# Kernel optimization log

Hardware: AMD Instinct MI355X
Metric: run time of the kernel (lower is better)

## Reference

```python
import jax, jax.numpy as jnp
import numpy as np

N_NODES = 100000
N_EDGES = 1600000


def setup_inputs() -> dict:
    key = jax.random.key(0)
    k1, k2, k3, k4 = jax.random.split(key, 4)
    x = jax.random.normal(k1, (N_NODES, 128), dtype=jnp.float32)
    edge_idx = jax.random.randint(k2, (2, N_EDGES), 0, N_NODES, dtype=jnp.int64)
    W1 = jax.random.normal(k3, (128, 64), dtype=jnp.float32) * (1.0 / np.sqrt(128))
    b1 = jnp.zeros((64,), dtype=jnp.float32)
    W2 = jax.random.normal(k4, (64, 40), dtype=jnp.float32) * (1.0 / np.sqrt(64))
    b2 = jnp.zeros((40,), dtype=jnp.float32)
    return {"x": x, "edge_idx": edge_idx, "W1": W1, "b1": b1, "W2": W2, "b2": b2}


def _gcn_conv(x, src, dst, norm, W, b, n_nodes):
    # x @ W -> gather by src, scale by symmetric norm, scatter-add to dst, + bias
    h = x @ W                               # [N, d_out]
    msg = h[src] * norm[:, None]            # [E+N, d_out]
    out = jax.ops.segment_sum(msg, dst, num_segments=n_nodes)
    return out + b


def _norm_and_loops(edge_idx, n_nodes):
    # PyG GCNConv default: add self-loops, norm = deg^-1/2[src] * deg^-1/2[dst]
    loops = jnp.arange(n_nodes, dtype=edge_idx.dtype)
    src = jnp.concatenate([edge_idx[0], loops])
    dst = jnp.concatenate([edge_idx[1], loops])
    deg = jnp.zeros((n_nodes,), jnp.float32).at[dst].add(1.0)
    dinv = jnp.where(deg > 0, jax.lax.rsqrt(deg), 0.0)
    norm = dinv[src] * dinv[dst]
    return src, dst, norm


def reference(x, edge_idx, W1, b1, W2, b2):
    n_nodes = x.shape[0]
    src, dst, norm = _norm_and_loops(edge_idx, n_nodes)
    hidden = jax.nn.relu(_gcn_conv(x, src, dst, norm, W1, b1, n_nodes))
    # dropout is a no-op in eval mode (training=False)
    return _gcn_conv(hidden, src, dst, norm, W2, b2, n_nodes)
```

## Files before the change

kernel.cpp:

```cpp
#include <hip/hip_runtime.h>

#define D_IN  128
#define D_HID 64
#define D_OUT 40

static __device__ __forceinline__ unsigned short f2bf(float f) {
    unsigned int u = __float_as_uint(f);
    unsigned int r = (u + 0x7fffu + ((u >> 16) & 1u)) >> 16;
    return (unsigned short)r;
}
static __device__ __forceinline__ float bflo(unsigned int u) {
    return __uint_as_float(u << 16);
}
static __device__ __forceinline__ float bfhi(unsigned int u) {
    return __uint_as_float(u & 0xffff0000u);
}

__global__ __launch_bounds__(256) void k_deg_g1(const int* __restrict__ dst,
                                                unsigned int* __restrict__ cnt,
                                                unsigned int* __restrict__ rank, int E, int DB,
                                                const float* __restrict__ x,
                                                const float* __restrict__ W1,
                                                unsigned short* __restrict__ h1s, int N) {
    __shared__ float w[D_IN * D_HID];
    __shared__ float xs[16][D_IN + 4];
    if ((int)blockIdx.x < DB) {
        int e = blockIdx.x * 256 + threadIdx.x;
        if (e < E) rank[e] = atomicAdd(&cnt[dst[e]], 1u);
        return;
    }
    const int tid = threadIdx.x;
    const float4* W4 = (const float4*)W1;
    float4* w4 = (float4*)w;
    for (int i = tid; i < D_IN * D_HID / 4; i += 256) w4[i] = W4[i];
    const int row0 = (blockIdx.x - DB) * 16;
    const float4* X4 = (const float4*)(x + (size_t)row0 * D_IN);
    for (int i = tid; i < 16 * D_IN / 4; i += 256) {
        float4 v = X4[i];
        int r = i >> 5;
        int k = (i & 31) * 4;
        *(float4*)&xs[r][k] = v;
    }
    __syncthreads();
    const int r  = tid >> 4;
    const int c4 = (tid & 15) * 4;
    float a0 = 0, a1 = 0, a2 = 0, a3 = 0;
#pragma unroll 8
    for (int k = 0; k < D_IN; ++k) {
        float  xv = xs[r][k];
        float4 wv = *(const float4*)&w[k * D_HID + c4];
        a0 = fmaf(xv, wv.x, a0);
        a1 = fmaf(xv, wv.y, a1);
        a2 = fmaf(xv, wv.z, a2);
        a3 = fmaf(xv, wv.w, a3);
    }
    const int row = row0 + r;
    if (row < N) {
        uint2 o;
        o.x = (unsigned)f2bf(a0) | ((unsigned)f2bf(a1) << 16);
        o.y = (unsigned)f2bf(a2) | ((unsigned)f2bf(a3) << 16);
        *(uint2*)&h1s[(size_t)row * D_HID + c4] = o;
    }
}

__global__ __launch_bounds__(256) void k_scan1(const unsigned int* __restrict__ deg,
                                               unsigned int* __restrict__ off,
                                               unsigned int* __restrict__ bsum,
                                               float* __restrict__ dinv, int N) {
    __shared__ unsigned int s[256];
    const int tid = threadIdx.x;
    const int i = blockIdx.x * 256 + tid;
    unsigned int v = (i < N) ? deg[i] : 0u;
    if (i < N) dinv[i] = rsqrtf((float)(v + 1u));
    s[tid] = v;
    __syncthreads();
    for (int d = 1; d < 256; d <<= 1) {
        unsigned int t = (tid >= d) ? s[tid - d] : 0u;
        __syncthreads();
        s[tid] += t;
        __syncthreads();
    }
    if (i < N) off[i] = s[tid] - v;
    if (tid == 255) bsum[blockIdx.x] = s[tid];
}

__global__ __launch_bounds__(512) void k_scan2(unsigned int* __restrict__ bsum, int NB) {
    __shared__ unsigned int s[512];
    const int tid = threadIdx.x;
    unsigned int v = (tid < NB) ? bsum[tid] : 0u;
    s[tid] = v;
    __syncthreads();
    for (int d = 1; d < 512; d <<= 1) {
        unsigned int t = (tid >= d) ? s[tid - d] : 0u;
        __syncthreads();
        s[tid] += t;
        __syncthreads();
    }
    if (tid < NB) bsum[tid] = s[tid] - v;
}

__global__ __launch_bounds__(256) void k_scan3(unsigned int* __restrict__ off,
                                               const unsigned int* __restrict__ bsum,
                                               int N, int E) {
    int i = blockIdx.x * 256 + threadIdx.x;
    if (i < N) off[i] += bsum[blockIdx.x];
    if (i == 0) off[N] = (unsigned int)E;
}

__global__ __launch_bounds__(256) void k_fill(const int* __restrict__ src,
                                              const int* __restrict__ dst,
                                              const unsigned int* __restrict__ off,
                                              const unsigned int* __restrict__ rank,
                                              int* __restrict__ csr_src, int E) {
    int e = blockIdx.x * 256 + threadIdx.x;
    if (e >= E) return;
    csr_src[off[dst[e]] + rank[e]] = src[e];
}

__global__ __launch_bounds__(256) void k_g1g2(const unsigned int* __restrict__ off,
                                              const int* __restrict__ csr_src,
                                              const unsigned int* __restrict__ h1s,
                                              const float* __restrict__ dinv,
                                              const float* __restrict__ b1,
                                              const float* __restrict__ W2,
                                              unsigned short* __restrict__ h2s, int N) {
    __shared__ float w2s[D_HID * D_OUT];
    __shared__ float hrow[8][D_HID];
    const int tid = threadIdx.x;
    const float4* W4 = (const float4*)W2;
    float4* w4 = (float4*)w2s;
    for (int i = tid; i < D_HID * D_OUT / 4; i += 256) w4[i] = W4[i];
    __syncthreads();

    const int lane = tid & 63;
    const int half = lane >> 5;
    const int hl   = lane & 31;
    const int slot = (tid >> 6) * 2 + half;
    const int node = blockIdx.x * 8 + slot;
    const bool valid = node < N;

    int start = 0, end = 0;
    float a0 = 0.0f, a1 = 0.0f;
    float dn = 0.0f;
    if (valid) {
        start = (int)off[node];
        end   = (int)off[node + 1];
        dn = dinv[node];
        unsigned int u = h1s[(size_t)node * 32 + hl];
        a0 = dn * bflo(u);
        a1 = dn * bfhi(u);
    }
    for (int base = start; base < end; base += 32) {
        const int nb = min(32, end - base);
        int sv = (base + hl < end) ? csr_src[base + hl] : 0;
        int j = 0;
        for (; j + 3 < nb; j += 4) {
            int s0 = __shfl(sv, j, 32),     s1 = __shfl(sv, j + 1, 32);
            int s2 = __shfl(sv, j + 2, 32), s3 = __shfl(sv, j + 3, 32);
            unsigned int u0 = h1s[(size_t)s0 * 32 + hl]; float d0 = dinv[s0];
            unsigned int u1 = h1s[(size_t)s1 * 32 + hl]; float d1 = dinv[s1];
            unsigned int u2 = h1s[(size_t)s2 * 32 + hl]; float d2 = dinv[s2];
            unsigned int u3 = h1s[(size_t)s3 * 32 + hl]; float d3 = dinv[s3];
            a0 = fmaf(d0, bflo(u0), a0); a1 = fmaf(d0, bfhi(u0), a1);
            a0 = fmaf(d1, bflo(u1), a0); a1 = fmaf(d1, bfhi(u1), a1);
            a0 = fmaf(d2, bflo(u2), a0); a1 = fmaf(d2, bfhi(u2), a1);
            a0 = fmaf(d3, bflo(u3), a0); a1 = fmaf(d3, bfhi(u3), a1);
        }
        for (; j < nb; ++j) {
            int s = __shfl(sv, j, 32);
            unsigned int uu = h1s[(size_t)s * 32 + hl];
            float dd = dinv[s];
            a0 = fmaf(dd, bflo(uu), a0);
            a1 = fmaf(dd, bfhi(uu), a1);
        }
    }
    if (valid) {
        const float2 bb = *(const float2*)&b1[hl * 2];
        float v0 = fmaf(dn, a0, bb.x);
        float v1 = fmaf(dn, a1, bb.y);
        hrow[slot][hl * 2]     = v0 > 0.0f ? v0 : 0.0f;
        hrow[slot][hl * 2 + 1] = v1 > 0.0f ? v1 : 0.0f;
    }
    __syncthreads();
    if (valid && hl < 20) {
        const int c2 = hl * 2;
        float s0 = 0.0f, s1 = 0.0f;
#pragma unroll 8
        for (int k = 0; k < D_HID; ++k) {
            float  xv = hrow[slot][k];
            float2 wv = *(const float2*)&w2s[k * D_OUT + c2];
            s0 = fmaf(xv, wv.x, s0);
            s1 = fmaf(xv, wv.y, s1);
        }
        unsigned int o = (unsigned)f2bf(s0 * dn) | ((unsigned)f2bf(s1 * dn) << 16);
        *(unsigned int*)&h2s[(size_t)node * D_OUT + c2] = o;
    }
}

__global__ __launch_bounds__(256) void k_gather2(const unsigned int* __restrict__ off,
                                                 const int* __restrict__ csr_src,
                                                 const unsigned int* __restrict__ h2s,
                                                 const float* __restrict__ dinv,
                                                 const float* __restrict__ b2,
                                                 float* __restrict__ out, int N) {
    const int gtid = blockIdx.x * 256 + threadIdx.x;
    const int wid2 = gtid >> 6;
    const int lane = threadIdx.x & 63;
    const int half = lane >> 5;
    const int hl   = lane & 31;
    const int node = wid2 * 2 + half;
    if (node >= N) return;
    const int start = (int)off[node];
    const int end   = (int)off[node + 1];
    const bool act = hl < 20;
    float a0 = 0.0f, a1 = 0.0f;
    if (act) {
        unsigned int u = h2s[(size_t)node * 20 + hl];
        a0 = bflo(u); a1 = bfhi(u);
    }
    for (int base = start; base < end; base += 32) {
        const int nb = min(32, end - base);
        int sv = (base + hl < end) ? csr_src[base + hl] : 0;
        int j = 0;
        for (; j + 3 < nb; j += 4) {
            int s0 = __shfl(sv, j, 32),     s1 = __shfl(sv, j + 1, 32);
            int s2 = __shfl(sv, j + 2, 32), s3 = __shfl(sv, j + 3, 32);
            if (act) {
                unsigned int u0 = h2s[(size_t)s0 * 20 + hl];
                unsigned int u1 = h2s[(size_t)s1 * 20 + hl];
                unsigned int u2 = h2s[(size_t)s2 * 20 + hl];
                unsigned int u3 = h2s[(size_t)s3 * 20 + hl];
                a0 += (bflo(u0) + bflo(u1)) + (bflo(u2) + bflo(u3));
                a1 += (bfhi(u0) + bfhi(u1)) + (bfhi(u2) + bfhi(u3));
            }
        }
        for (; j < nb; ++j) {
            int s = __shfl(sv, j, 32);
            if (act) {
                unsigned int uu = h2s[(size_t)s * 20 + hl];
                a0 += bflo(uu);
                a1 += bfhi(uu);
            }
        }
    }
    if (act) {
        const float dv = dinv[node];
        const float2 bb = *(const float2*)&b2[hl * 2];
        float2 o = {fmaf(dv, a0, bb.x), fmaf(dv, a1, bb.y)};
        *(float2*)&out[(size_t)node * D_OUT + hl * 2] = o;
    }
}

extern "C" void kernel_launch(void* const* d_in, const int* in_sizes, int n_in,
                              void* d_out, int out_size, void* d_ws, size_t ws_size,
                              hipStream_t stream) {
    const float* x  = (const float*)d_in[0];
    const int*  eix = (const int*)d_in[1];
    const float* W1 = (const float*)d_in[2];
    const float* b1 = (const float*)d_in[3];
    const float* W2 = (const float*)d_in[4];
    const float* b2 = (const float*)d_in[5];
    float* out = (float*)d_out;

    const int N = in_sizes[0] / D_IN;
    const int E = in_sizes[1] / 2;
    const int* src = eix;
    const int* dst = eix + E;
    const int NB = (N + 255) / 256;

    char* ws = (char*)d_ws;
    size_t off_b = 0;
    auto alloc = [&](size_t bytes) {
        void* p = ws + off_b;
        off_b = (off_b + bytes + 255) & ~(size_t)255;
        return p;
    };
    unsigned int*   deg     = (unsigned int*)alloc((size_t)N * 4);
    float*          dinv    = (float*)alloc((size_t)N * 4);
    unsigned int*   offsets = (unsigned int*)alloc((size_t)(N + 1) * 4);
    unsigned int*   bsums   = (unsigned int*)alloc(512 * 4);
    int*            csr_src = (int*)alloc((size_t)E * 4);
    unsigned short* h1s     = (unsigned short*)alloc((size_t)N * D_HID * 2);
    unsigned short* h2s     = (unsigned short*)alloc((size_t)E >= (size_t)N * D_OUT / 2
                                                     ? (size_t)E * 4 : (size_t)N * D_OUT * 2);
    unsigned int*   rank    = (unsigned int*)h2s;

    hipMemsetAsync(deg, 0, (size_t)N * 4, stream);

    const int DB = (E + 255) / 256;
    const int GB = (N + 15) / 16;

    k_deg_g1<<<DB + GB, 256, 0, stream>>>(dst, deg, rank, E, DB, x, W1, h1s, N);

    k_scan1<<<NB, 256, 0, stream>>>(deg, offsets, bsums, dinv, N);
    k_scan2<<<1, 512, 0, stream>>>(bsums, NB);
    k_scan3<<<NB, 256, 0, stream>>>(offsets, bsums, N, E);
    k_fill <<<(E + 255) / 256, 256, 0, stream>>>(src, dst, offsets, rank, csr_src, E);

    k_g1g2  <<<(N + 7) / 8, 256, 0, stream>>>(offsets, csr_src, (const unsigned int*)h1s,
                                              dinv, b1, W2, h2s, N);
    const int gwaves = (N + 1) / 2;
    const int gblocks = (gwaves + 3) / 4;
    k_gather2<<<gblocks, 256, 0, stream>>>(offsets, csr_src, (const unsigned int*)h2s,
                                           dinv, b2, out, N);
}
```

Measured before the change: 328.2 us.

## Prescale layer-1 features by source dinv to drop per-edge dinv gathers

The degree-count and GEMM1 kernels are split apart so GEMM1 runs after dinv is known. Each row of h1 is then multiplied by its source node's inverse-sqrt degree before the bf16 store. This removes the random per-edge dinv loads and multiplies from the layer-1 gather, which becomes a plain sum. The cost is losing the overlap of the atomic degree pass with the GEMM, plus a serialization point and a slight change in bf16 rounding.

Measured after the change: 338.1 us. 1.03x slower.

```diff
diff --git a/kernel.cpp b/kernel.cpp
--- a/kernel.cpp
+++ b/kernel.cpp
@@ -16,24 +16,78 @@
     return __uint_as_float(u & 0xffff0000u);
 }
 
-__global__ __launch_bounds__(256) void k_deg_g1(const int* __restrict__ dst,
-                                                unsigned int* __restrict__ cnt,
-                                                unsigned int* __restrict__ rank, int E, int DB,
-                                                const float* __restrict__ x,
-                                                const float* __restrict__ W1,
-                                                unsigned short* __restrict__ h1s, int N) {
+__global__ __launch_bounds__(256) void k_deg(const int* __restrict__ dst,
+                                             unsigned int* __restrict__ cnt,
+                                             unsigned int* __restrict__ rank, int E) {
+    int e = blockIdx.x * 256 + threadIdx.x;
+    if (e < E) rank[e] = atomicAdd(&cnt[dst[e]], 1u);
+}
+
+__global__ __launch_bounds__(256) void k_scan1(const unsigned int* __restrict__ deg,
+                                               unsigned int* __restrict__ off,
+                                               unsigned int* __restrict__ bsum,
+                                               float* __restrict__ dinv, int N) {
+    __shared__ unsigned int s[256];
+    const int tid = threadIdx.x;
+    const int i = blockIdx.x * 256 + tid;
+    unsigned int v = (i < N) ? deg[i] : 0u;
+    if (i < N) dinv[i] = rsqrtf((float)(v + 1u));
+    s[tid] = v;
+    __syncthreads();
+    for (int d = 1; d < 256; d <<= 1) {
+        unsigned int t = (tid >= d) ? s[tid - d] : 0u;
+        __syncthreads();
+        s[tid] += t;
+        __syncthreads();
+    }
+    if (i < N) off[i] = s[tid] - v;
+    if (tid == 255) bsum[blockIdx.x] = s[tid];
+}
+
+__global__ __launch_bounds__(512) void k_scan2(unsigned int* __restrict__ bsum, int NB) {
+    __shared__ unsigned int s[512];
+    const int tid = threadIdx.x;
+    unsigned int v = (tid < NB) ? bsum[tid] : 0u;
+    s[tid] = v;
+    __syncthreads();
+    for (int d = 1; d < 512; d <<= 1) {
+        unsigned int t = (tid >= d) ? s[tid - d] : 0u;
+        __syncthreads();
+        s[tid] += t;
+        __syncthreads();
+    }
+    if (tid < NB) bsum[tid] = s[tid] - v;
+}
+
+__global__ __launch_bounds__(256) void k_scan3(unsigned int* __restrict__ off,
+                                               const unsigned int* __restrict__ bsum,
+                                               int N, int E) {
+    int i = blockIdx.x * 256 + threadIdx.x;
+    if (i < N) off[i] += bsum[blockIdx.x];
+    if (i == 0) off[N] = (unsigned int)E;
+}
+
+__global__ __launch_bounds__(256) void k_fill(const int* __restrict__ src,
+                                              const int* __restrict__ dst,
+                                              const unsigned int* __restrict__ off,
+                                              const unsigned int* __restrict__ rank,
+                                              int* __restrict__ csr_src, int E) {
+    int e = blockIdx.x * 256 + threadIdx.x;
+    if (e >= E) return;
+    csr_src[off[dst[e]] + rank[e]] = src[e];
+}
+
+__global__ __launch_bounds__(256) void k_gemm1(const float* __restrict__ x,
+                                               const float* __restrict__ W1,
+                                               const float* __restrict__ dinv,
+                                               unsigned short* __restrict__ h1s, int N) {
     __shared__ float w[D_IN * D_HID];
     __shared__ float xs[16][D_IN + 4];
-    if ((int)blockIdx.x < DB) {
-        int e = blockIdx.x * 256 + threadIdx.x;
-        if (e < E) rank[e] = atomicAdd(&cnt[dst[e]], 1u);
-        return;
-    }
     const int tid = threadIdx.x;
     const float4* W4 = (const float4*)W1;
     float4* w4 = (float4*)w;
     for (int i = tid; i < D_IN * D_HID / 4; i += 256) w4[i] = W4[i];
-    const int row0 = (blockIdx.x - DB) * 16;
+    const int row0 = blockIdx.x * 16;
     const float4* X4 = (const float4*)(x + (size_t)row0 * D_IN);
     for (int i = tid; i < 16 * D_IN / 4; i += 256) {
         float4 v = X4[i];
@@ -56,65 +110,12 @@
     }
     const int row = row0 + r;
     if (row < N) {
+        float dv = dinv[row];
         uint2 o;
-        o.x = (unsigned)f2bf(a0) | ((unsigned)f2bf(a1) << 16);
-        o.y = (unsigned)f2bf(a2) | ((unsigned)f2bf(a3) << 16);
+        o.x = (unsigned)f2bf(a0 * dv) | ((unsigned)f2bf(a1 * dv) << 16);
+        o.y = (unsigned)f2bf(a2 * dv) | ((unsigned)f2bf(a3 * dv) << 16);
         *(uint2*)&h1s[(size_t)row * D_HID + c4] = o;
     }
-}
-
-__global__ __launch_bounds__(256) void k_scan1(const unsigned int* __restrict__ deg,
-                                               unsigned int* __restrict__ off,
-                                               unsigned int* __restrict__ bsum,
-                                               float* __restrict__ dinv, int N) {
-    __shared__ unsigned int s[256];
-    const int tid = threadIdx.x;
-    const int i = blockIdx.x * 256 + tid;
-    unsigned int v = (i < N) ? deg[i] : 0u;
-    if (i < N) dinv[i] = rsqrtf((float)(v + 1u));
-    s[tid] = v;
-    __syncthreads();
-    for (int d = 1; d < 256; d <<= 1) {
-        unsigned int t = (tid >= d) ? s[tid - d] : 0u;
-        __syncthreads();
-        s[tid] += t;
-        __syncthreads();
-    }
-    if (i < N) off[i] = s[tid] - v;
-    if (tid == 255) bsum[blockIdx.x] = s[tid];
-}
-
-__global__ __launch_bounds__(512) void k_scan2(unsigned int* __restrict__ bsum, int NB) {
-    __shared__ unsigned int s[512];
-    const int tid = threadIdx.x;
-    unsigned int v = (tid < NB) ? bsum[tid] : 0u;
-    s[tid] = v;
-    __syncthreads();
-    for (int d = 1; d < 512; d <<= 1) {
-        unsigned int t = (tid >= d) ? s[tid - d] : 0u;
-        __syncthreads();
-        s[tid] += t;
-        __syncthreads();
-    }
-    if (tid < NB) bsum[tid] = s[tid] - v;
-}
-
-__global__ __launch_bounds__(256) void k_scan3(unsigned int* __restrict__ off,
-                                               const unsigned int* __restrict__ bsum,
-                                               int N, int E) {
-    int i = blockIdx.x * 256 + threadIdx.x;
-    if (i < N) off[i] += bsum[blockIdx.x];
-    if (i == 0) off[N] = (unsigned int)E;
-}
-
-__global__ __launch_bounds__(256) void k_fill(const int* __restrict__ src,
-                                              const int* __restrict__ dst,
-                                              const unsigned int* __restrict__ off,
-                                              const unsigned int* __restrict__ rank,
-                                              int* __restrict__ csr_src, int E) {
-    int e = blockIdx.x * 256 + threadIdx.x;
-    if (e >= E) return;
-    csr_src[off[dst[e]] + rank[e]] = src[e];
 }
 
 __global__ __launch_bounds__(256) void k_g1g2(const unsigned int* __restrict__ off,
@@ -140,15 +141,14 @@
     const bool valid = node < N;
 
     int start = 0, end = 0;
-    float a0 = 0.0f, a1 = 0.0f;
-    float dn = 0.0f;
+    float a0 = 0.0f, a1 = 0.0f, dn = 0.0f;
     if (valid) {
         start = (int)off[node];
         end   = (int)off[node + 1];
         dn = dinv[node];
         unsigned int u = h1s[(size_t)node * 32 + hl];
-        a0 = dn * bflo(u);
-        a1 = dn * bfhi(u);
+        a0 = bflo(u);
+        a1 = bfhi(u);
     }
     for (int base = start; base < end; base += 32) {
         const int nb = min(32, end - base);
@@ -157,21 +157,18 @@
         for (; j + 3 < nb; j += 4) {
             int s0 = __shfl(sv, j, 32),     s1 = __shfl(sv, j + 1, 32);
             int s2 = __shfl(sv, j + 2, 32), s3 = __shfl(sv, j + 3, 32);
-            unsigned int u0 = h1s[(size_t)s0 * 32 + hl]; float d0 = dinv[s0];
-            unsigned int u1 = h1s[(size_t)s1 * 32 + hl]; float d1 = dinv[s1];
-            unsigned int u2 = h1s[(size_t)s2 * 32 + hl]; float d2 = dinv[s2];
-            unsigned int u3 = h1s[(size_t)s3 * 32 + hl]; float d3 = dinv[s3];
-            a0 = fmaf(d0, bflo(u0), a0); a1 = fmaf(d0, bfhi(u0), a1);
-            a0 = fmaf(d1, bflo(u1), a0); a1 = fmaf(d1, bfhi(u1), a1);
-            a0 = fmaf(d2, bflo(u2), a0); a1 = fmaf(d2, bfhi(u2), a1);
-            a0 = fmaf(d3, bflo(u3), a0); a1 = fmaf(d3, bfhi(u3), a1);
+            unsigned int u0 = h1s[(size_t)s0 * 32 + hl];
+            unsigned int u1 = h1s[(size_t)s1 * 32 + hl];
+            unsigned int u2 = h1s[(size_t)s2 * 32 + hl];
+            unsigned int u3 = h1s[(size_t)s3 * 32 + hl];
+            a0 += (bflo(u0) + bflo(u1)) + (bflo(u2) + bflo(u3));
+            a1 += (bfhi(u0) + bfhi(u1)) + (bfhi(u2) + bfhi(u3));
         }
         for (; j < nb; ++j) {
             int s = __shfl(sv, j, 32);
             unsigned int uu = h1s[(size_t)s * 32 + hl];
-            float dd = dinv[s];
-            a0 = fmaf(dd, bflo(uu), a0);
-            a1 = fmaf(dd, bfhi(uu), a1);
+            a0 += bflo(uu);
+            a1 += bfhi(uu);
         }
     }
     if (valid) {
@@ -287,14 +284,12 @@
 
     hipMemsetAsync(deg, 0, (size_t)N * 4, stream);
 
-    const int DB = (E + 255) / 256;
-    const int GB = (N + 15) / 16;
-
-    k_deg_g1<<<DB + GB, 256, 0, stream>>>(dst, deg, rank, E, DB, x, W1, h1s, N);
-
+    k_deg  <<<(E + 255) / 256, 256, 0, stream>>>(dst, deg, rank, E);
     k_scan1<<<NB, 256, 0, stream>>>(deg, offsets, bsums, dinv, N);
     k_scan2<<<1, 512, 0, stream>>>(bsums, NB);
     k_scan3<<<NB, 256, 0, stream>>>(offsets, bsums, N, E);
+
+    k_gemm1<<<(N + 15) / 16, 256, 0, stream>>>(x, W1, dinv, h1s, N);
     k_fill <<<(E + 255) / 256, 256, 0, stream>>>(src, dst, offsets, rank, csr_src, E);
 
     k_g1g2  <<<(N + 7) / 8, 256, 0, stream>>>(offsets, csr_src, (const unsigned int*)h1s,
```
